# Optimization experiments

Measured on AMD Instinct MI355X. Metric: run time of the kernel, lower is better.

The kernel has to match this reference:

```python
import jax, jax.numpy as jnp
import numpy as np

D_MODEL = 512
NUM_HEADS = 8
D_HEAD = D_MODEL // NUM_HEADS


def setup_inputs() -> dict:
    key = jax.random.key(0)
    ks = jax.random.split(key, 16)
    B, S, D, H, dh = 8, 1024, D_MODEL, NUM_HEADS, D_HEAD
    s = 1.0 / np.sqrt(D)
    return {
        "query": jax.random.normal(ks[0], (B, S, D), jnp.float32),
        "key": jax.random.normal(ks[1], (B, S, D), jnp.float32),
        "value": jax.random.normal(ks[2], (B, S, D), jnp.float32),
        "pos_emb": jax.random.normal(ks[3], (B, S, D), jnp.float32),
        "Wq": jax.random.normal(ks[4], (D, D), jnp.float32) * s,
        "bq": jnp.zeros((D,), jnp.float32),
        "Wk": jax.random.normal(ks[5], (D, D), jnp.float32) * s,
        "bk": jnp.zeros((D,), jnp.float32),
        "Wv": jax.random.normal(ks[6], (D, D), jnp.float32) * s,
        "bv": jnp.zeros((D,), jnp.float32),
        "Wpos": jax.random.normal(ks[7], (D, D), jnp.float32) * s,  # pos_proj has no bias
        "Wo": jax.random.normal(ks[8], (D, D), jnp.float32) * s,
        "bo": jnp.zeros((D,), jnp.float32),
        "u_bias": jax.random.normal(ks[9], (H, dh), jnp.float32) * 0.02,
        "v_bias": jax.random.normal(ks[10], (H, dh), jnp.float32) * 0.02,
    }


def _rel_shift(x):
    # x: [B, H, S, S] -> Transformer-XL relative shift
    B, H, S1, S2 = x.shape
    x = jnp.pad(x, ((0, 0), (0, 0), (0, 0), (1, 0)))  # zero col at front
    x = x.reshape(B, H, S2 + 1, S1)[:, :, 1:, :]
    return x.reshape(B, H, S1, S2)


def reference(query, key, value, pos_emb, Wq, bq, Wk, bk, Wv, bv, Wpos, Wo, bo, u_bias, v_bias):
    B, S, D = query.shape
    H, dh = NUM_HEADS, D_HEAD
    q = (query @ Wq + bq).reshape(B, S, H, dh)      # [B,S,H,dh]
    k = (key @ Wk + bk).reshape(B, S, H, dh)
    v = (value @ Wv + bv).reshape(B, S, H, dh)
    p = (pos_emb @ Wpos).reshape(B, S, H, dh)
    content_score = jnp.einsum('bqhd,bkhd->bhqk', q + u_bias, k)
    pos_score = _rel_shift(jnp.einsum('bqhd,bkhd->bhqk', q + v_bias, p))
    score = (content_score + pos_score) / jnp.sqrt(jnp.float32(D))
    attn = jax.nn.softmax(score, axis=-1)
    ctx = jnp.einsum('bhqk,bkhd->bqhd', attn, v).reshape(B, S, D)
    return ctx @ Wo + bo
```

## Files before the change

### kernel.cpp

```cpp
#include <hip/hip_runtime.h>
#include <hip/hip_bf16.h>

typedef unsigned short u16;
typedef unsigned int u32;
typedef __attribute__((ext_vector_type(4))) float f32x4;
typedef __attribute__((ext_vector_type(8))) short s16x8;
typedef __attribute__((ext_vector_type(4))) short s16x4;

#define DEV static __device__ __forceinline__

DEV u16 f2bf(float f){ return __builtin_bit_cast(u16, __float2bfloat16(f)); }
DEV float bf2f(u16 v){ union{u32 u;float f;}x; x.u = ((u32)v)<<16; return x.f; }
DEV float bitsf(u32 u){ union{u32 u;float f;}x; x.u = u; return x.f; }

DEV f32x4 MF(s16x8 a, s16x8 b, f32x4 c){ return __builtin_amdgcn_mfma_f32_16x16x32_bf16(a,b,c,0,0,0); }

DEV s16x8 frag64(const u16* lds, int row, int slot){
  return *(const s16x8*)(lds + row*64 + ((slot ^ (row&7))<<3));
}

__global__ __launch_bounds__(256) void k_prep(
  const float* __restrict__ Wq, const float* __restrict__ Wk, const float* __restrict__ Wv,
  const float* __restrict__ Wp, const float* __restrict__ Wo, u16* __restrict__ WT)
{
  const int bx = blockIdx.x; const int mat = bx>>6, tile = bx&63;
  const float* W = (mat==0)?Wq:(mat==1)?Wk:(mat==2)?Wv:(mat==3)?Wp:Wo;
  u16* dst = WT + mat*262144;
  const int k0 = (tile>>3)<<6, n0 = (tile&7)<<6;
  __shared__ u16 L[64*68];
  const int t = threadIdx.x;
#pragma unroll
  for (int i=0;i<4;i++){
    int id = t + 256*i; int row = id>>4, c4 = (id&15)<<2;
    float4 v = *(const float4*)(W + (k0+row)*512 + n0 + c4);
    s16x4 o; o[0]=(short)f2bf(v.x); o[1]=(short)f2bf(v.y); o[2]=(short)f2bf(v.z); o[3]=(short)f2bf(v.w);
    *(s16x4*)(L + row*68 + c4) = o;
  }
  __syncthreads();
#pragma unroll
  for (int i=0;i<2;i++){
    int id = t + 256*i; int nl = id>>3, slot = id&7;
    s16x8 v;
#pragma unroll
    for (int j=0;j<8;j++) v[j] = (short)L[(slot*8+j)*68 + nl];
    *(s16x8*)(dst + (n0+nl)*512 + k0 + slot*8) = v;
  }
}

__global__ __launch_bounds__(256,2) void k_proj(
  const float* __restrict__ Xq, const float* __restrict__ Xk,
  const float* __restrict__ Xv, const float* __restrict__ Xp,
  const u16* __restrict__ WT,
  const float* __restrict__ bq, const float* __restrict__ bk, const float* __restrict__ bv,
  const float* __restrict__ ub, const float* __restrict__ vb,
  u16* __restrict__ Qu, u16* __restrict__ Qv, u16* __restrict__ Kb,
  u16* __restrict__ Pb, u16* __restrict__ Vt)
{
  const int job = blockIdx.z;
  const float* X = (job==0)?Xq:(job==1)?Xk:(job==2)?Xp:Xv;
  const int wsel = (job==0)?0:(job==1)?1:(job==2)?3:2;
  const u16* W = WT + wsel*262144;
  const int m0 = blockIdx.y*128, n0 = blockIdx.x*128;
  __shared__ u16 As[128*64];
  __shared__ u16 Bs[128*64];
  const int t = threadIdx.x, lane = t&63, w = t>>6;
  const int wm = w&1, wn = w>>1;
  f32x4 acc[4][4];
#pragma unroll
  for (int i=0;i<4;i++)
#pragma unroll
    for (int j=0;j<4;j++) acc[i][j] = (f32x4){0.f,0.f,0.f,0.f};

  for (int kt=0; kt<8; ++kt){
    const int k0 = kt*64;
    __syncthreads();
#pragma unroll
    for (int i=0;i<8;i++){
      int id = t + 256*i; int row = id>>4; int c4 = (id&15)<<2;
      float4 v = *(const float4*)(X + (m0+row)*512 + k0 + c4);
      s16x4 o; o[0]=(short)f2bf(v.x); o[1]=(short)f2bf(v.y); o[2]=(short)f2bf(v.z); o[3]=(short)f2bf(v.w);
      *(s16x4*)(As + row*64 + ((((c4>>3)^(row&7))<<3) + (c4&4))) = o;
    }
#pragma unroll
    for (int i=0;i<4;i++){
      int id = t + 256*i; int row = id>>3, slot = id&7;
      s16x8 v = *(const s16x8*)(W + (n0+row)*512 + k0 + slot*8);
      *(s16x8*)(Bs + row*64 + ((slot^(row&7))<<3)) = v;
    }
    __syncthreads();
#pragma unroll
    for (int kk=0;kk<2;kk++){
      const int slotk = kk*4 + (lane>>4);
      s16x8 xf[4], wf[4];
#pragma unroll
      for (int j=0;j<4;j++){ int r = wm*64 + j*16 + (lane&15); xf[j] = frag64(As, r, slotk); }
#pragma unroll
      for (int i=0;i<4;i++){ int r = wn*64 + i*16 + (lane&15); wf[i] = frag64(Bs, r, slotk); }
      if (job != 3){
#pragma unroll
        for (int i=0;i<4;i++)
#pragma unroll
          for (int j=0;j<4;j++) acc[i][j] = MF(wf[i], xf[j], acc[i][j]);
      } else {
#pragma unroll
        for (int i=0;i<4;i++)
#pragma unroll
          for (int j=0;j<4;j++) acc[i][j] = MF(xf[i], wf[j], acc[i][j]);
      }
    }
  }

  const int b = m0>>10;
  if (job != 3){
#pragma unroll
    for (int i=0;i<4;i++){
      const int n = n0 + wn*64 + i*16 + ((lane>>4)<<2);
      const int hh = n>>6, d = n&63;
      f32x4 b1 = {0.f,0.f,0.f,0.f}, b2 = {0.f,0.f,0.f,0.f};
      if (job==0){
        f32x4 q4 = *(const f32x4*)(bq+n); f32x4 u4 = *(const f32x4*)(ub+n); f32x4 v4 = *(const f32x4*)(vb+n);
        b1 = q4 + u4; b2 = q4 + v4;
      } else if (job==1){
        b1 = *(const f32x4*)(bk+n);
      }
#pragma unroll
      for (int j=0;j<4;j++){
        const int m = m0 + wm*64 + j*16 + (lane&15);
        const int s = m&1023;
        const int off = ((b*8+hh)*1024 + s)*64 + d;
        f32x4 a = acc[i][j];
        s16x4 o1;
#pragma unroll
        for (int r=0;r<4;r++) o1[r] = (short)f2bf(a[r]+b1[r]);
        if (job==0){
          *(s16x4*)(Qu+off) = o1;
          s16x4 o2;
#pragma unroll
          for (int r=0;r<4;r++) o2[r] = (short)f2bf(a[r]+b2[r]);
          *(s16x4*)(Qv+off) = o2;
        } else if (job==1) *(s16x4*)(Kb+off) = o1;
        else               *(s16x4*)(Pb+off) = o1;
      }
    }
  } else {
#pragma unroll
    for (int j=0;j<4;j++){
      const int n = n0 + wn*64 + j*16 + (lane&15);
      const int hh = n>>6, d = n&63;
      const float bvn = bv[n];
#pragma unroll
      for (int i=0;i<4;i++){
        const int m = m0 + wm*64 + i*16 + ((lane>>4)<<2);
        const int s = m&1023;
        f32x4 a = acc[i][j];
        s16x4 o;
#pragma unroll
        for (int r=0;r<4;r++) o[r] = (short)f2bf(a[r]+bvn);
        *(s16x4*)(Vt + ((b*8+hh)*64 + d)*1024 + s) = o;
      }
    }
  }
}

#define SC_SLOT(q, slot) ((((slot)) & ~7) | ((((slot))&7) ^ ((q)&7)))

__global__ __launch_bounds__(512,4) void k_attn(
  const u16* __restrict__ Qu, const u16* __restrict__ Qv,
  const u16* __restrict__ Kb, const u16* __restrict__ Pb,
  const u16* __restrict__ Vt, u16* __restrict__ Ctx)
{
  const int qb = blockIdx.x, h = blockIdx.y, b = blockIdx.z;
  const int q0 = qb*32;
  const int bh = b*8 + h;
  const u16* Qu_ = Qu + bh*65536;
  const u16* Qv_ = Qv + bh*65536;
  const u16* Kb_ = Kb + bh*65536;
  const u16* Pb_ = Pb + bh*65536;
  const u16* Vt_ = Vt + bh*65536;
  u16* Ctx_ = Ctx + bh*65536;
  __shared__ u16 sc[33*1024];
  __shared__ u16 Ts[64*64];
  __shared__ float stats[32];
  const int t = threadIdx.x, lane = t&63, w = t>>6;
  const int l15 = lane&15, lg = lane>>4;
  const int qband = w&1, sub = w>>1;
  const int qi = qband*16 + l15;
  const int q  = q0 + qi;
  const int srow = t>>3, sslot = t&7;
  u16* tsw = Ts + srow*64 + ((sslot^(srow&7))<<3);
  const u16* srcP = Pb_ + srow*64 + sslot*8;
  const u16* srcK = Kb_ + srow*64 + sslot*8;
  const u16* srcV = Vt_ + srow*1024 + sslot*8;

  const int priBand = w>>2, jtp = w&3;
  s16x8 qvp[2], qvb2[2];
#pragma unroll
  for (int kk=0;kk<2;kk++){
    qvp[kk]  = *(const s16x8*)(Qv_ + (q0 + priBand*16 + l15)*64 + (kk*4+lg)*8);
    int r2 = q0 + 17 + l15; if (r2 > 1023) r2 = 1023;
    qvb2[kk] = *(const s16x8*)(Qv_ + r2*64 + (kk*4+lg)*8);
  }

  {
    s16x8 p0 = *(const s16x8*)(srcP);
    s16x8 p1 = *(const s16x8*)(srcP + 4096);
    for (int u=0; u<16; ++u){
      __syncthreads();
      *(s16x8*)tsw = p0;
      p0 = p1;
      if (u+2<16) p1 = *(const s16x8*)(srcP + (u+2)*4096);
      __syncthreads();
      {
        f32x4 ps = {0.f,0.f,0.f,0.f};
#pragma unroll
        for (int kk=0;kk<2;kk++){
          s16x8 pf = frag64(Ts, jtp*16 + l15, kk*4+lg);
          ps = MF(pf, qvp[kk], ps);
        }
        const int prow = priBand*16 + l15;
        const int j0 = u*64 + jtp*16 + lg*4;
        s16x4 o;
#pragma unroll
        for (int r=0;r<4;r++) o[r] = (short)f2bf(ps[r]);
        *(s16x4*)(sc + prow*1024 + ((((j0>>2) ^ ((prow&15)<<1)))<<2)) = o;
      }
      if ((u&1) == (w>>2)){
        f32x4 ps = {0.f,0.f,0.f,0.f};
#pragma unroll
        for (int kk=0;kk<2;kk++){
          s16x8 pf = frag64(Ts, (w&3)*16 + l15, kk*4+lg);
          ps = MF(pf, qvb2[kk], ps);
        }
        if (l15 == 15){
          const int j0 = u*64 + (w&3)*16 + lg*4;
          s16x4 o;
#pragma unroll
          for (int r=0;r<4;r++) o[r] = (short)f2bf(ps[r]);
          *(s16x4*)(sc + 32*1024 + ((j0>>2)<<2)) = o;
        }
      }
    }
  }

  __syncthreads();

  u32 stash[32];
#pragma unroll
  for (int kt=0; kt<16; ++kt){
#pragma unroll
    for (int rp=0; rp<2; ++rp){
      u32 wv = 0;
#pragma unroll
      for (int hh=0; hh<2; ++hh){
        const int k = kt*64 + sub*16 + lg*4 + rp*2 + hh;
        const int above = (k > q) ? 1 : 0;
        int jj = above ? (k - q - 2) : (1023 - q + k);
        const bool zero = (k == q+1);
        if (jj < 0) jj = 0;
        const int row = qi + above;
        const int addr = row*1024 + ((((jj>>2) ^ ((row&15)<<1)))<<2) + (jj&3);
        u32 v = zero ? 0u : (u32)sc[addr];
        wv |= v << (16*hh);
      }
      stash[kt*2+rp] = wv;
    }
  }

  s16x8 qfu[2];
#pragma unroll
  for (int kk=0;kk<2;kk++)
    qfu[kk] = *(const s16x8*)(Qu_ + q*64 + (kk*4+lg)*8);

  {
    s16x8 k0r = *(const s16x8*)(srcK);
    s16x8 k1r = *(const s16x8*)(srcK + 4096);
    for (int kt=0; kt<16; ++kt){
      __syncthreads();
      *(s16x8*)tsw = k0r;
      k0r = k1r;
      if (kt+2<16) k1r = *(const s16x8*)(srcK + (kt+2)*4096);
      __syncthreads();
      f32x4 a = {0.f,0.f,0.f,0.f};
#pragma unroll
      for (int kk=0;kk<2;kk++){
        s16x8 kf = frag64(Ts, sub*16 + l15, kk*4+lg);
        a = MF(kf, qfu[kk], a);
      }
      const int kb2 = kt*64 + sub*16 + lg*4;
      const u32 w0 = stash[kt*2], w1 = stash[kt*2+1];
      const float p0 = bitsf(w0<<16), p1 = bitsf(w0 & 0xffff0000u);
      const float p2 = bitsf(w1<<16), p3 = bitsf(w1 & 0xffff0000u);
      s16x4 o;
      o[0]=(short)f2bf(a[0]+p0); o[1]=(short)f2bf(a[1]+p1);
      o[2]=(short)f2bf(a[2]+p2); o[3]=(short)f2bf(a[3]+p3);
      *(s16x4*)(sc + qi*1024 + SC_SLOT(qi, kb2>>3)*8 + (kb2&4)) = o;
    }
  }

  __syncthreads();

  {
    const int row = t>>4, c = t&15;
    float mx = -1e30f;
#pragma unroll
    for (int i=0;i<8;i++){
      const int slot = c + 16*i;
      s16x8 v = *(const s16x8*)(sc + row*1024 + SC_SLOT(row,slot)*8);
#pragma unroll
      for (int j2=0;j2<8;j2++) mx = fmaxf(mx, bf2f((u16)v[j2]));
    }
    mx = fmaxf(mx, __shfl_xor(mx,1));
    mx = fmaxf(mx, __shfl_xor(mx,2));
    mx = fmaxf(mx, __shfl_xor(mx,4));
    mx = fmaxf(mx, __shfl_xor(mx,8));
    float sum = 0.f;
    const float SCALE = 0.044194173824159216f;
#pragma unroll
    for (int i=0;i<8;i++){
      const int slot = c + 16*i;
      u16* p = sc + row*1024 + SC_SLOT(row,slot)*8;
      s16x8 v = *(const s16x8*)p;
      s16x8 o;
#pragma unroll
      for (int j2=0;j2<8;j2++){
        float e = __expf((bf2f((u16)v[j2]) - mx)*SCALE);
        sum += e; o[j2] = (short)f2bf(e);
      }
      *(s16x8*)p = o;
    }
    sum += __shfl_xor(sum,1); sum += __shfl_xor(sum,2);
    sum += __shfl_xor(sum,4); sum += __shfl_xor(sum,8);
    if (c==0) stats[row] = 1.0f/sum;
  }

  f32x4 accC = {0.f,0.f,0.f,0.f};
  {
    s16x8 v0r = *(const s16x8*)(srcV);
    s16x8 v1r = *(const s16x8*)(srcV + 64);
    for (int kt=0; kt<16; ++kt){
      __syncthreads();
      *(s16x8*)tsw = v0r;
      v0r = v1r;
      if (kt+2<16) v1r = *(const s16x8*)(srcV + (kt+2)*64);
      __syncthreads();
#pragma unroll
      for (int kk=0;kk<2;kk++){
        const int slotk = kk*4 + lg;
        s16x8 vf = frag64(Ts, sub*16 + l15, slotk);
        const int slot = kt*8 + slotk;
        s16x8 pfr = *(const s16x8*)(sc + qi*1024 + SC_SLOT(qi,slot)*8);
        accC = MF(vf, pfr, accC);
      }
    }
  }
  {
    const float inv = stats[qi];
    const int d0 = sub*16 + lg*4;
    s16x4 o;
#pragma unroll
    for (int r=0;r<4;r++) o[r] = (short)f2bf(accC[r]*inv);
    *(s16x4*)(Ctx_ + (q0+qi)*64 + d0) = o;
  }
}

__global__ __launch_bounds__(256,2) void k_out(
  const u16* __restrict__ Ctx, const u16* __restrict__ WT,
  const float* __restrict__ bo, float* __restrict__ Out)
{
  const u16* W = WT + 4*262144;
  const int m0 = blockIdx.y*128, n0 = blockIdx.x*128;
  const int b = m0>>10, s0 = m0&1023;
  __shared__ u16 As[128*64];
  __shared__ u16 Bs[128*64];
  const int t = threadIdx.x, lane = t&63, w = t>>6;
  const int wm = w&1, wn = w>>1;
  f32x4 acc[4][4];
#pragma unroll
  for (int i=0;i<4;i++)
#pragma unroll
    for (int j=0;j<4;j++) acc[i][j] = (f32x4){0.f,0.f,0.f,0.f};

  for (int kt=0; kt<8; ++kt){
    const int k0 = kt*64, hh = kt;
    __syncthreads();
#pragma unroll
    for (int i=0;i<4;i++){
      int id = t + 256*i; int row = id>>3, slot = id&7;
      s16x8 v = *(const s16x8*)(Ctx + ((b*8+hh)*1024 + s0 + row)*64 + slot*8);
      *(s16x8*)(As + row*64 + ((slot^(row&7))<<3)) = v;
    }
#pragma unroll
    for (int i=0;i<4;i++){
      int id = t + 256*i; int row = id>>3, slot = id&7;
      s16x8 v = *(const s16x8*)(W + (n0+row)*512 + k0 + slot*8);
      *(s16x8*)(Bs + row*64 + ((slot^(row&7))<<3)) = v;
    }
    __syncthreads();
#pragma unroll
    for (int kk=0;kk<2;kk++){
      const int slotk = kk*4 + (lane>>4);
      s16x8 xf[4], wf[4];
#pragma unroll
      for (int j=0;j<4;j++){ int r = wm*64 + j*16 + (lane&15); xf[j] = frag64(As, r, slotk); }
#pragma unroll
      for (int i=0;i<4;i++){ int r = wn*64 + i*16 + (lane&15); wf[i] = frag64(Bs, r, slotk); }
#pragma unroll
      for (int i=0;i<4;i++)
#pragma unroll
        for (int j=0;j<4;j++) acc[i][j] = MF(wf[i], xf[j], acc[i][j]);
    }
  }
#pragma unroll
  for (int i=0;i<4;i++){
    const int n = n0 + wn*64 + i*16 + ((lane>>4)<<2);
    f32x4 bo4 = *(const f32x4*)(bo + n);
#pragma unroll
    for (int j=0;j<4;j++){
      const int m = m0 + wm*64 + j*16 + (lane&15);
      f32x4 o = acc[i][j] + bo4;
      *(f32x4*)(Out + m*512 + n) = o;
    }
  }
}

extern "C" void kernel_launch(void* const* d_in, const int* in_sizes, int n_in,
                              void* d_out, int out_size, void* d_ws, size_t ws_size,
                              hipStream_t stream)
{
  const float* query = (const float*)d_in[0];
  const float* key   = (const float*)d_in[1];
  const float* value = (const float*)d_in[2];
  const float* pos   = (const float*)d_in[3];
  const float* Wq = (const float*)d_in[4];
  const float* bq = (const float*)d_in[5];
  const float* Wk = (const float*)d_in[6];
  const float* bk = (const float*)d_in[7];
  const float* Wv = (const float*)d_in[8];
  const float* bv = (const float*)d_in[9];
  const float* Wp = (const float*)d_in[10];
  const float* Wo = (const float*)d_in[11];
  const float* bo = (const float*)d_in[12];
  const float* ub = (const float*)d_in[13];
  const float* vb = (const float*)d_in[14];
  float* Out = (float*)d_out;

  u16* ws  = (u16*)d_ws;
  u16* WT  = ws;
  u16* Qu  = ws + 1310720;
  u16* Qv  = Qu + 4194304;
  u16* Kb  = Qv + 4194304;
  u16* Pb  = Kb + 4194304;
  u16* Vt  = Pb + 4194304;
  u16* Ctx = Vt + 4194304;

  k_prep<<<dim3(320),      dim3(256), 0, stream>>>(Wq,Wk,Wv,Wp,Wo,WT);
  k_proj<<<dim3(4,64,4),   dim3(256), 0, stream>>>(query,key,value,pos,WT,bq,bk,bv,ub,vb,Qu,Qv,Kb,Pb,Vt);
  k_attn<<<dim3(32,8,8),   dim3(512), 0, stream>>>(Qu,Qv,Kb,Pb,Vt,Ctx);
  k_out<<<dim3(4,64),      dim3(256), 0, stream>>>(Ctx,WT,bo,Out);
}
```

Measured before the change: 186.3 us.

## Remap grids for XCD-local L2 reuse, fuse row max into score pass, pad LDS

k_proj and k_attn now launch as flat 1D grids whose block index is decoded so that blocks sharing the same head or row tile land on the same XCD. This is meant to improve L2 reuse of K/P/V and input tiles. k_attn keeps a running max during score generation and stores it in a partial-max array, so softmax no longer re-reads LDS to find the row max. Softmax switches to exp2 with a fused multiply-add. The score buffer rows are padded to 1032 to reduce bank conflicts, and the tile loops are fully unrolled. The launch-bounds occupancy hint drops from 4 to 2 and the PV d-tile index now comes from w>>1; that index equals the old sub, so it is a cosmetic rename rather than a new split.

```diff
diff --git a/kernel.cpp b/kernel.cpp
--- a/kernel.cpp
+++ b/kernel.cpp
@@ -56,11 +56,14 @@
   u16* __restrict__ Qu, u16* __restrict__ Qv, u16* __restrict__ Kb,
   u16* __restrict__ Pb, u16* __restrict__ Vt)
 {
-  const int job = blockIdx.z;
+  const int Lb = blockIdx.x;
+  const int xcd = Lb & 7, li = Lb >> 3;
+  const int n0  = (li & 3) * 128;
+  const int job = (li >> 2) & 3;
+  const int m0  = (xcd*8 + (li >> 4)) * 128;
   const float* X = (job==0)?Xq:(job==1)?Xk:(job==2)?Xp:Xv;
   const int wsel = (job==0)?0:(job==1)?1:(job==2)?3:2;
   const u16* W = WT + wsel*262144;
-  const int m0 = blockIdx.y*128, n0 = blockIdx.x*128;
   __shared__ u16 As[128*64];
   __shared__ u16 Bs[128*64];
   const int t = threadIdx.x, lane = t&63, w = t>>6;
@@ -162,24 +165,28 @@
   }
 }
 
+#define SCS 1032
 #define SC_SLOT(q, slot) ((((slot)) & ~7) | ((((slot))&7) ^ ((q)&7)))
 
-__global__ __launch_bounds__(512,4) void k_attn(
+__global__ __launch_bounds__(512,2) void k_attn(
   const u16* __restrict__ Qu, const u16* __restrict__ Qv,
   const u16* __restrict__ Kb, const u16* __restrict__ Pb,
   const u16* __restrict__ Vt, u16* __restrict__ Ctx)
 {
-  const int qb = blockIdx.x, h = blockIdx.y, b = blockIdx.z;
+  const int Lb = blockIdx.x;
+  const int xcd = Lb & 7, li = Lb >> 3;
+  const int bh = xcd*8 + (li>>5);
+  const int qb = li & 31;
   const int q0 = qb*32;
-  const int bh = b*8 + h;
   const u16* Qu_ = Qu + bh*65536;
   const u16* Qv_ = Qv + bh*65536;
   const u16* Kb_ = Kb + bh*65536;
   const u16* Pb_ = Pb + bh*65536;
   const u16* Vt_ = Vt + bh*65536;
   u16* Ctx_ = Ctx + bh*65536;
-  __shared__ u16 sc[33*1024];
-  __shared__ u16 Ts[64*64];
+  __shared__ u16 sc[33*SCS];
+  __shared__ u16 Ts[4096];
+  __shared__ float pmax[512];
   __shared__ float stats[32];
   const int t = threadIdx.x, lane = t&63, w = t>>6;
   const int l15 = lane&15, lg = lane>>4;
@@ -204,6 +211,7 @@
   {
     s16x8 p0 = *(const s16x8*)(srcP);
     s16x8 p1 = *(const s16x8*)(srcP + 4096);
+#pragma unroll
     for (int u=0; u<16; ++u){
       __syncthreads();
       *(s16x8*)tsw = p0;
@@ -222,7 +230,7 @@
         s16x4 o;
 #pragma unroll
         for (int r=0;r<4;r++) o[r] = (short)f2bf(ps[r]);
-        *(s16x4*)(sc + prow*1024 + ((((j0>>2) ^ ((prow&15)<<1)))<<2)) = o;
+        *(s16x4*)(sc + prow*SCS + ((((j0>>2) ^ ((prow&15)<<1)))<<2)) = o;
       }
       if ((u&1) == (w>>2)){
         f32x4 ps = {0.f,0.f,0.f,0.f};
@@ -236,7 +244,7 @@
           s16x4 o;
 #pragma unroll
           for (int r=0;r<4;r++) o[r] = (short)f2bf(ps[r]);
-          *(s16x4*)(sc + 32*1024 + ((j0>>2)<<2)) = o;
+          *(s16x4*)(sc + 32*SCS + ((j0>>2)<<2)) = o;
         }
       }
     }
@@ -258,7 +266,7 @@
         const bool zero = (k == q+1);
         if (jj < 0) jj = 0;
         const int row = qi + above;
-        const int addr = row*1024 + ((((jj>>2) ^ ((row&15)<<1)))<<2) + (jj&3);
+        const int addr = row*SCS + ((((jj>>2) ^ ((row&15)<<1)))<<2) + (jj&3);
         u32 v = zero ? 0u : (u32)sc[addr];
         wv |= v << (16*hh);
       }
@@ -271,9 +279,11 @@
   for (int kk=0;kk<2;kk++)
     qfu[kk] = *(const s16x8*)(Qu_ + q*64 + (kk*4+lg)*8);
 
+  float rmax = -1e30f;
   {
     s16x8 k0r = *(const s16x8*)(srcK);
     s16x8 k1r = *(const s16x8*)(srcK + 4096);
+#pragma unroll
     for (int kt=0; kt<16; ++kt){
       __syncthreads();
       *(s16x8*)tsw = k0r;
@@ -288,42 +298,40 @@
       }
       const int kb2 = kt*64 + sub*16 + lg*4;
       const u32 w0 = stash[kt*2], w1 = stash[kt*2+1];
-      const float p0 = bitsf(w0<<16), p1 = bitsf(w0 & 0xffff0000u);
-      const float p2 = bitsf(w1<<16), p3 = bitsf(w1 & 0xffff0000u);
+      const float v0 = a[0] + bitsf(w0<<16);
+      const float v1 = a[1] + bitsf(w0 & 0xffff0000u);
+      const float v2 = a[2] + bitsf(w1<<16);
+      const float v3 = a[3] + bitsf(w1 & 0xffff0000u);
+      rmax = fmaxf(rmax, fmaxf(fmaxf(v0,v1), fmaxf(v2,v3)));
       s16x4 o;
-      o[0]=(short)f2bf(a[0]+p0); o[1]=(short)f2bf(a[1]+p1);
-      o[2]=(short)f2bf(a[2]+p2); o[3]=(short)f2bf(a[3]+p3);
-      *(s16x4*)(sc + qi*1024 + SC_SLOT(qi, kb2>>3)*8 + (kb2&4)) = o;
-    }
-  }
+      o[0]=(short)f2bf(v0); o[1]=(short)f2bf(v1);
+      o[2]=(short)f2bf(v2); o[3]=(short)f2bf(v3);
+      *(s16x4*)(sc + qi*SCS + SC_SLOT(qi, kb2>>3)*8 + (kb2&4)) = o;
+    }
+  }
+  pmax[qi*16 + sub*4 + lg] = rmax;
 
   __syncthreads();
 
   {
     const int row = t>>4, c = t&15;
-    float mx = -1e30f;
-#pragma unroll
-    for (int i=0;i<8;i++){
-      const int slot = c + 16*i;
-      s16x8 v = *(const s16x8*)(sc + row*1024 + SC_SLOT(row,slot)*8);
-#pragma unroll
-      for (int j2=0;j2<8;j2++) mx = fmaxf(mx, bf2f((u16)v[j2]));
-    }
+    float mx = pmax[row*16 + c];
     mx = fmaxf(mx, __shfl_xor(mx,1));
     mx = fmaxf(mx, __shfl_xor(mx,2));
     mx = fmaxf(mx, __shfl_xor(mx,4));
     mx = fmaxf(mx, __shfl_xor(mx,8));
+    const float S2 = 0.063762029f;
+    const float nm = -mx * S2;
     float sum = 0.f;
-    const float SCALE = 0.044194173824159216f;
 #pragma unroll
     for (int i=0;i<8;i++){
       const int slot = c + 16*i;
-      u16* p = sc + row*1024 + SC_SLOT(row,slot)*8;
+      u16* p = sc + row*SCS + SC_SLOT(row,slot)*8;
       s16x8 v = *(const s16x8*)p;
       s16x8 o;
 #pragma unroll
       for (int j2=0;j2<8;j2++){
-        float e = __expf((bf2f((u16)v[j2]) - mx)*SCALE);
+        float e = exp2f(__builtin_fmaf(bf2f((u16)v[j2]), S2, nm));
         sum += e; o[j2] = (short)f2bf(e);
       }
       *(s16x8*)p = o;
@@ -334,9 +342,11 @@
   }
 
   f32x4 accC = {0.f,0.f,0.f,0.f};
+  const int dtile = w>>1;
   {
     s16x8 v0r = *(const s16x8*)(srcV);
     s16x8 v1r = *(const s16x8*)(srcV + 64);
+#pragma unroll
     for (int kt=0; kt<16; ++kt){
       __syncthreads();
       *(s16x8*)tsw = v0r;
@@ -346,16 +356,16 @@
 #pragma unroll
       for (int kk=0;kk<2;kk++){
         const int slotk = kk*4 + lg;
-        s16x8 vf = frag64(Ts, sub*16 + l15, slotk);
+        s16x8 vf = frag64(Ts, dtile*16 + l15, slotk);
         const int slot = kt*8 + slotk;
-        s16x8 pfr = *(const s16x8*)(sc + qi*1024 + SC_SLOT(qi,slot)*8);
+        s16x8 pfr = *(const s16x8*)(sc + qi*SCS + SC_SLOT(qi,slot)*8);
         accC = MF(vf, pfr, accC);
       }
     }
   }
   {
     const float inv = stats[qi];
-    const int d0 = sub*16 + lg*4;
+    const int d0 = dtile*16 + lg*4;
     s16x4 o;
 #pragma unroll
     for (int r=0;r<4;r++) o[r] = (short)f2bf(accC[r]*inv);
@@ -453,8 +463,8 @@
   u16* Vt  = Pb + 4194304;
   u16* Ctx = Vt + 4194304;
 
-  k_prep<<<dim3(320),      dim3(256), 0, stream>>>(Wq,Wk,Wv,Wp,Wo,WT);
-  k_proj<<<dim3(4,64,4),   dim3(256), 0, stream>>>(query,key,value,pos,WT,bq,bk,bv,ub,vb,Qu,Qv,Kb,Pb,Vt);
-  k_attn<<<dim3(32,8,8),   dim3(512), 0, stream>>>(Qu,Qv,Kb,Pb,Vt,Ctx);
-  k_out<<<dim3(4,64),      dim3(256), 0, stream>>>(Ctx,WT,bo,Out);
-}
+  k_prep<<<dim3(320),  dim3(256), 0, stream>>>(Wq,Wk,Wv,Wp,Wo,WT);
+  k_proj<<<dim3(1024), dim3(256), 0, stream>>>(query,key,value,pos,WT,bq,bk,bv,ub,vb,Qu,Qv,Kb,Pb,Vt);
+  k_attn<<<dim3(2048), dim3(512), 0, stream>>>(Qu,Qv,Kb,Pb,Vt,Ctx);
+  k_out<<<dim3(4,64),  dim3(256), 0, stream>>>(Ctx,WT,bo,Out);
+}
```

New measurement: 205.9 us. 1.11x slower.
